# Kernel tuning notes

Hardware: AMD Instinct MI355X
Metric: run time of the kernel (lower is better)

The kernel has to match this reference:

```python
import jax, jax.numpy as jnp
import numpy as np


def setup_inputs() -> dict:
    key = jax.random.key(0)
    k1, k2 = jax.random.split(key)
    B, S, N, M = 4, 4, 4096, 4096
    output_points = jax.random.normal(k1, (B, S, N, 3), dtype=jnp.float32)
    target_points = jax.random.normal(k2, (B, S, M, 3), dtype=jnp.float32)
    return {"output_points": output_points, "target_points": target_points, "n_samples": 4096}


def reference(output_points, target_points, n_samples):
    # output_points: [B,S,N,3], target_points: [B,S,M,3] (already sampled to n_samples pts)
    x2 = jnp.sum(output_points * output_points, axis=-1)  # [B,S,N]
    y2 = jnp.sum(target_points * target_points, axis=-1)  # [B,S,M]
    xy = jnp.einsum('bsnd,bsmd->bsnm', output_points, target_points)  # [B,S,N,M]
    # squared pairwise distances; clamp tiny negatives from fp error
    d2 = jnp.maximum(x2[..., :, None] + y2[..., None, :] - 2.0 * xy, 0.0)
    dist1 = jnp.min(d2, axis=-1)  # [B,S,N] NN dist output->target (squared)
    dist2 = jnp.min(d2, axis=-2)  # [B,S,M] NN dist target->output (squared)
    # dist_combined per (b,s) = mean(dist1) + mean(dist2); tensor is [S,B]
    chamfer = jnp.mean(dist1, axis=-1) + jnp.mean(dist2, axis=-1)  # [B,S]
    return chamfer.T  # [n_future_steps, batch_size]
```

## Files before the change

### kernel.cpp

```cpp
#include <hip/hip_runtime.h>


constexpr int B = 4, S = 4, NPTS = 4096, PAIRS = B * S;
constexpr int THREADS = 1024;
constexpr int WAVES = THREADS / 64;
constexpr int QPT = 8;
constexpr int QPB = 64 * QPT;
constexpr int QTILES = NPTS / QPB;
constexpr int SEG = NPTS / WAVES;

typedef float v2f __attribute__((ext_vector_type(2)));

#define PK_FMA_ZW(g, q, rzw)                                              \
  asm("v_pk_fma_f32 %0, %1, %2, %2 op_sel:[0,0,1] op_sel_hi:[1,0,1]"      \
      : "=v"(g) : "v"(q), "v"(rzw))
#define PK_FMA_Y(g, q, rxy)                                               \
  asm("v_pk_fma_f32 %0, %1, %2, %0 op_sel:[0,1,0] op_sel_hi:[1,1,1]"      \
      : "+v"(g) : "v"(q), "v"(rxy))
#define PK_FMA_X(g, q, rxy)                                               \
  asm("v_pk_fma_f32 %0, %1, %2, %0 op_sel:[0,0,0] op_sel_hi:[1,0,1]"      \
      : "+v"(g) : "v"(q), "v"(rxy))

__global__ __launch_bounds__(THREADS, 4)
void chamfer_pk3_kernel(const float* __restrict__ out_pts,
                        const float* __restrict__ tgt_pts,
                        float* __restrict__ out) {
  const int t     = threadIdx.x;
  const int l     = t & 63;
  const int wid   = t >> 6;
  const int qtile = blockIdx.x;
  const int pair  = blockIdx.y;
  const int dir   = blockIdx.z;

  const float* qbase = (dir == 0 ? out_pts : tgt_pts) + (size_t)pair * NPTS * 3;
  const float* rbase = (dir == 0 ? tgt_pts : out_pts) + (size_t)pair * NPTS * 3;

  __shared__ float4 sref[NPTS];

  #pragma unroll
  for (int k = 0; k < NPTS / THREADS; ++k) {
    const int i = t + k * THREADS;
    const float rx = rbase[3 * i], ry = rbase[3 * i + 1], rz = rbase[3 * i + 2];
    sref[i] = make_float4(rx, ry, rz, -0.5f * (rx * rx + ry * ry + rz * rz));
  }

  v2f qx[4], qy[4], qz[4];
  #pragma unroll
  for (int p = 0; p < 4; ++p) {
    const int q0 = qtile * QPB + (2 * p) * 64 + l;
    const int q1 = q0 + 64;
    qx[p] = v2f{qbase[3 * q0], qbase[3 * q1]};
    qy[p] = v2f{qbase[3 * q0 + 1], qbase[3 * q1 + 1]};
    qz[p] = v2f{qbase[3 * q0 + 2], qbase[3 * q1 + 2]};
  }

  float acc[QPT];
  #pragma unroll
  for (int j = 0; j < QPT; ++j) acc[j] = -3.0e38f;

  __syncthreads();

  const int base = wid * SEG;
  #pragma unroll 2
  for (int r = 0; r < SEG; r += 2) {
    const float4 rf0 = sref[base + r];
    const float4 rf1 = sref[base + r + 1];
    v2f rxy0; rxy0.x = rf0.x; rxy0.y = rf0.y;
    v2f rzw0; rzw0.x = rf0.z; rzw0.y = rf0.w;
    v2f rxy1; rxy1.x = rf1.x; rxy1.y = rf1.y;
    v2f rzw1; rzw1.x = rf1.z; rzw1.y = rf1.w;
    #pragma unroll
    for (int p = 0; p < 4; ++p) {
      v2f g0, g1;
      PK_FMA_ZW(g0, qz[p], rzw0);
      PK_FMA_Y (g0, qy[p], rxy0);
      PK_FMA_X (g0, qx[p], rxy0);
      PK_FMA_ZW(g1, qz[p], rzw1);
      PK_FMA_Y (g1, qy[p], rxy1);
      PK_FMA_X (g1, qx[p], rxy1);
      acc[2 * p]     = fmaxf(fmaxf(acc[2 * p], g0.x), g1.x);
      acc[2 * p + 1] = fmaxf(fmaxf(acc[2 * p + 1], g0.y), g1.y);
    }
  }

  __syncthreads();
  float* Sf = reinterpret_cast<float*>(sref);

  #pragma unroll
  for (int j = 0; j < QPT; ++j) Sf[wid * QPB + j * 64 + l] = acc[j];
  __syncthreads();

  if (t < QPB) {
    float g = Sf[t];
    #pragma unroll
    for (int w = 1; w < WAVES; ++w) g = fmaxf(g, Sf[w * QPB + t]);
    const int j = t >> 6, p = j >> 1, h = j & 1;
    const float x2 = qx[p][h] * qx[p][h] + qy[p][h] * qy[p][h] + qz[p][h] * qz[p][h];
    float d = fmaxf(fmaf(-2.0f, g, x2), 0.0f);
    #pragma unroll
    for (int off = 1; off < 64; off <<= 1) d += __shfl_xor(d, off, 64);
    if (l == 0) Sf[WAVES * QPB + (t >> 6)] = d;
  }
  __syncthreads();
  if (t == 0) {
    float ssum = 0.0f;
    #pragma unroll
    for (int w = 0; w < QPB / 64; ++w) ssum += Sf[WAVES * QPB + w];
    const int b = pair >> 2, s = pair & 3;
    atomicAdd(&out[s * B + b], ssum * (1.0f / NPTS));
  }
}

extern "C" void kernel_launch(void* const* d_in, const int* in_sizes, int n_in,
                              void* d_out, int out_size, void* d_ws, size_t ws_size,
                              hipStream_t stream) {
  const float* out_pts = (const float*)d_in[0];
  const float* tgt_pts = (const float*)d_in[1];
  float* out = (float*)d_out;

  hipMemsetAsync(out, 0, out_size * sizeof(float), stream);
  dim3 grid(QTILES, PAIRS, 2);
  chamfer_pk3_kernel<<<grid, THREADS, 0, stream>>>(out_pts, tgt_pts, out);
}
```

Baseline: 99.23 us.

## Compute pairwise dot products with bf16 split-precision MFMA and two-pass reduction

Replaces the packed-FP32 VALU inner loop with 16x16x32 bf16 MFMA instructions. Each coordinate is split into three bf16 terms (hi/mid/lo) so the products approximate fp32 accuracy, and the -0.5*|r|^2 term is folded into the K dimension. Reference points are also split into four chunks across blocks; per-chunk maxima go to a workspace and a second finalize kernel combines them. This trades VALU FMA throughput for matrix-core throughput, at the cost of an extra launch, workspace traffic, and possible precision loss from the bf16 splitting.

```diff
diff --git a/kernel.cpp b/kernel.cpp
--- a/kernel.cpp
+++ b/kernel.cpp
@@ -2,110 +2,188 @@
 
 
 constexpr int B = 4, S = 4, NPTS = 4096, PAIRS = B * S;
-constexpr int THREADS = 1024;
+constexpr int UNITS = PAIRS * 2;
+constexpr int THREADS = 512;
 constexpr int WAVES = THREADS / 64;
-constexpr int QPT = 8;
-constexpr int QPB = 64 * QPT;
-constexpr int QTILES = NPTS / QPB;
-constexpr int SEG = NPTS / WAVES;
-
-typedef float v2f __attribute__((ext_vector_type(2)));
-
-#define PK_FMA_ZW(g, q, rzw)                                              \
-  asm("v_pk_fma_f32 %0, %1, %2, %2 op_sel:[0,0,1] op_sel_hi:[1,0,1]"      \
-      : "=v"(g) : "v"(q), "v"(rzw))
-#define PK_FMA_Y(g, q, rxy)                                               \
-  asm("v_pk_fma_f32 %0, %1, %2, %0 op_sel:[0,1,0] op_sel_hi:[1,1,1]"      \
-      : "+v"(g) : "v"(q), "v"(rxy))
-#define PK_FMA_X(g, q, rxy)                                               \
-  asm("v_pk_fma_f32 %0, %1, %2, %0 op_sel:[0,0,0] op_sel_hi:[1,0,1]"      \
-      : "+v"(g) : "v"(q), "v"(rxy))
+constexpr int AFRAGS = 8;
+constexpr int QPB = WAVES * AFRAGS * 16;
+constexpr int QCH = NPTS / QPB;
+constexpr int RCH = 4;
+constexpr int RPB = NPTS / RCH;
+constexpr int RTILES = RPB / 16;
+constexpr unsigned short BF16_ONE = 0x3F80;
+
+typedef __attribute__((ext_vector_type(8))) short bf16x8;
+typedef __attribute__((ext_vector_type(4))) float f32x4;
+typedef __attribute__((ext_vector_type(4))) unsigned int u32x4;
+
+static __device__ inline unsigned short bf16_rne(float v) {
+  unsigned int u = __builtin_bit_cast(unsigned int, v);
+  u += 0x7FFFu + ((u >> 16) & 1u);
+  return (unsigned short)(u >> 16);
+}
+static __device__ inline float bf16f(unsigned short h) {
+  unsigned int u = (unsigned int)h << 16;
+  return __builtin_bit_cast(float, u);
+}
+static __device__ inline unsigned int bpack(unsigned short lo, unsigned short hi) {
+  return (unsigned int)lo | ((unsigned int)hi << 16);
+}
+
+struct Split3 { unsigned short h, m, l; };
+static __device__ inline Split3 split3(float v) {
+  Split3 s;
+  s.h = bf16_rne(v);
+  float r = v - bf16f(s.h);
+  s.m = bf16_rne(r);
+  r -= bf16f(s.m);
+  s.l = bf16_rne(r);
+  return s;
+}
+
 
 __global__ __launch_bounds__(THREADS, 4)
-void chamfer_pk3_kernel(const float* __restrict__ out_pts,
-                        const float* __restrict__ tgt_pts,
-                        float* __restrict__ out) {
-  const int t     = threadIdx.x;
-  const int l     = t & 63;
-  const int wid   = t >> 6;
-  const int qtile = blockIdx.x;
-  const int pair  = blockIdx.y;
-  const int dir   = blockIdx.z;
-
-  const float* qbase = (dir == 0 ? out_pts : tgt_pts) + (size_t)pair * NPTS * 3;
-  const float* rbase = (dir == 0 ? tgt_pts : out_pts) + (size_t)pair * NPTS * 3;
-
-  __shared__ float4 sref[NPTS];
-
-  #pragma unroll
-  for (int k = 0; k < NPTS / THREADS; ++k) {
-    const int i = t + k * THREADS;
-    const float rx = rbase[3 * i], ry = rbase[3 * i + 1], rz = rbase[3 * i + 2];
-    sref[i] = make_float4(rx, ry, rz, -0.5f * (rx * rx + ry * ry + rz * rz));
-  }
-
-  v2f qx[4], qy[4], qz[4];
-  #pragma unroll
-  for (int p = 0; p < 4; ++p) {
-    const int q0 = qtile * QPB + (2 * p) * 64 + l;
-    const int q1 = q0 + 64;
-    qx[p] = v2f{qbase[3 * q0], qbase[3 * q1]};
-    qy[p] = v2f{qbase[3 * q0 + 1], qbase[3 * q1 + 1]};
-    qz[p] = v2f{qbase[3 * q0 + 2], qbase[3 * q1 + 2]};
-  }
-
-  float acc[QPT];
-  #pragma unroll
-  for (int j = 0; j < QPT; ++j) acc[j] = -3.0e38f;
-
-  __syncthreads();
-
-  const int base = wid * SEG;
-  #pragma unroll 2
-  for (int r = 0; r < SEG; r += 2) {
-    const float4 rf0 = sref[base + r];
-    const float4 rf1 = sref[base + r + 1];
-    v2f rxy0; rxy0.x = rf0.x; rxy0.y = rf0.y;
-    v2f rzw0; rzw0.x = rf0.z; rzw0.y = rf0.w;
-    v2f rxy1; rxy1.x = rf1.x; rxy1.y = rf1.y;
-    v2f rzw1; rzw1.x = rf1.z; rzw1.y = rf1.w;
-    #pragma unroll
-    for (int p = 0; p < 4; ++p) {
-      v2f g0, g1;
-      PK_FMA_ZW(g0, qz[p], rzw0);
-      PK_FMA_Y (g0, qy[p], rxy0);
-      PK_FMA_X (g0, qx[p], rxy0);
-      PK_FMA_ZW(g1, qz[p], rzw1);
-      PK_FMA_Y (g1, qy[p], rxy1);
-      PK_FMA_X (g1, qx[p], rxy1);
-      acc[2 * p]     = fmaxf(fmaxf(acc[2 * p], g0.x), g1.x);
-      acc[2 * p + 1] = fmaxf(fmaxf(acc[2 * p + 1], g0.y), g1.y);
-    }
-  }
-
-  __syncthreads();
-  float* Sf = reinterpret_cast<float*>(sref);
-
-  #pragma unroll
-  for (int j = 0; j < QPT; ++j) Sf[wid * QPB + j * 64 + l] = acc[j];
-  __syncthreads();
-
-  if (t < QPB) {
-    float g = Sf[t];
-    #pragma unroll
-    for (int w = 1; w < WAVES; ++w) g = fmaxf(g, Sf[w * QPB + t]);
-    const int j = t >> 6, p = j >> 1, h = j & 1;
-    const float x2 = qx[p][h] * qx[p][h] + qy[p][h] * qy[p][h] + qz[p][h] * qz[p][h];
-    float d = fmaxf(fmaf(-2.0f, g, x2), 0.0f);
-    #pragma unroll
-    for (int off = 1; off < 64; off <<= 1) d += __shfl_xor(d, off, 64);
-    if (l == 0) Sf[WAVES * QPB + (t >> 6)] = d;
-  }
+void chamfer_mfma_main(const float* __restrict__ out_pts,
+                       const float* __restrict__ tgt_pts,
+                       float* __restrict__ part) {
+  const int t = threadIdx.x;
+  const int l = t & 63;
+  const int wid = t >> 6;
+  const int qc = blockIdx.x;
+  const int rc = blockIdx.y;
+  const int unit = blockIdx.z;
+  const int pair = unit >> 1, dir = unit & 1;
+
+  const float* qpts = (dir == 0 ? out_pts : tgt_pts) + (size_t)pair * NPTS * 3;
+  const float* rpts = (dir == 0 ? tgt_pts : out_pts) + (size_t)pair * NPTS * 3;
+
+  __shared__ u32x4 lds[RTILES * 64];
+
+  {
+    const int q0 = qc * QPB;
+    #pragma unroll
+    for (int rep = 0; rep < QPB / THREADS; ++rep) {
+      const int j = t + rep * THREADS;
+      const float x = qpts[3 * (q0 + j)];
+      const float y = qpts[3 * (q0 + j) + 1];
+      const float z = qpts[3 * (q0 + j) + 2];
+      const Split3 sx = split3(x), sy = split3(y), sz = split3(z);
+      u32x4* base = lds + (j >> 4) * 64 + (j & 15);
+      const u32x4 g0 = {bpack(sx.h, sx.h), bpack(sx.m, sx.h),
+                        bpack(sx.l, sx.m), bpack(sy.h, sy.h)};
+      const u32x4 g1 = {bpack(sy.m, sy.h), bpack(sy.l, sy.m),
+                        bpack(sz.h, sz.h), bpack(sz.m, sz.h)};
+      const u32x4 g2 = {bpack(sz.l, sz.m), bpack(BF16_ONE, BF16_ONE),
+                        bpack(BF16_ONE, 0), 0u};
+      const u32x4 g3 = {0u, 0u, 0u, 0u};
+      base[0] = g0; base[16] = g1; base[32] = g2; base[48] = g3;
+    }
+  }
+  __syncthreads();
+
+  bf16x8 a[AFRAGS];
+  #pragma unroll
+  for (int m = 0; m < AFRAGS; ++m)
+    a[m] = ((const bf16x8*)lds)[(wid * AFRAGS + m) * 64 + l];
+  __syncthreads();
+
+  {
+    const int r0 = rc * RPB;
+    #pragma unroll
+    for (int rep = 0; rep < RPB / THREADS; ++rep) {
+      const int j = t + rep * THREADS;
+      const float x = rpts[3 * (r0 + j)];
+      const float y = rpts[3 * (r0 + j) + 1];
+      const float z = rpts[3 * (r0 + j) + 2];
+      const float w = -0.5f * (x * x + y * y + z * z);
+      const Split3 sx = split3(x), sy = split3(y), sz = split3(z), sw = split3(w);
+      u32x4* base = lds + (j >> 4) * 64 + (j & 15);
+      const u32x4 g0 = {bpack(sx.h, sx.m), bpack(sx.h, sx.l),
+                        bpack(sx.h, sx.m), bpack(sy.h, sy.m)};
+      const u32x4 g1 = {bpack(sy.h, sy.l), bpack(sy.h, sy.m),
+                        bpack(sz.h, sz.m), bpack(sz.h, sz.l)};
+      const u32x4 g2 = {bpack(sz.h, sz.m), bpack(sw.h, sw.m),
+                        bpack(sw.l, 0), 0u};
+      const u32x4 g3 = {0u, 0u, 0u, 0u};
+      base[0] = g0; base[16] = g1; base[32] = g2; base[48] = g3;
+    }
+  }
+  __syncthreads();
+
+  f32x4 acc[AFRAGS];
+  #pragma unroll
+  for (int m = 0; m < AFRAGS; ++m)
+    acc[m] = (f32x4){-3.0e38f, -3.0e38f, -3.0e38f, -3.0e38f};
+
+  const f32x4 czero = {0.f, 0.f, 0.f, 0.f};
+  const bf16x8* bptr = (const bf16x8*)lds;
+  for (int tt = 0; tt < RTILES; tt += 2) {
+    const bf16x8 b0 = bptr[tt * 64 + l];
+    const bf16x8 b1 = bptr[(tt + 1) * 64 + l];
+    #pragma unroll
+    for (int m = 0; m < AFRAGS; ++m) {
+      const f32x4 d0 = __builtin_amdgcn_mfma_f32_16x16x32_bf16(a[m], b0, czero, 0, 0, 0);
+      const f32x4 d1 = __builtin_amdgcn_mfma_f32_16x16x32_bf16(a[m], b1, czero, 0, 0, 0);
+      #pragma unroll
+      for (int c = 0; c < 4; ++c)
+        acc[m][c] = fmaxf(fmaxf(acc[m][c], d0[c]), d1[c]);
+    }
+  }
+
+  #pragma unroll
+  for (int m = 0; m < AFRAGS; ++m) {
+    #pragma unroll
+    for (int c = 0; c < 4; ++c) {
+      float g = acc[m][c];
+      g = fmaxf(g, __shfl_xor(g, 1, 64));
+      g = fmaxf(g, __shfl_xor(g, 2, 64));
+      g = fmaxf(g, __shfl_xor(g, 4, 64));
+      g = fmaxf(g, __shfl_xor(g, 8, 64));
+      acc[m][c] = g;
+    }
+  }
+  const int jj = l & 15, hi = l >> 4;
+  float v_lo = 0.f, v_hi = 0.f;
+  #pragma unroll
+  for (int m = 0; m < 4; ++m) {
+    #pragma unroll
+    for (int c = 0; c < 4; ++c) {
+      const bool sel = (jj == m * 4 + c);
+      v_lo = sel ? acc[m][c] : v_lo;
+      v_hi = sel ? acc[m + 4][c] : v_hi;
+    }
+  }
+  const int q = qc * QPB + wid * (AFRAGS * 16) + (jj >> 2) * 16 + hi * 4 + (jj & 3);
+  float* pdst = part + ((size_t)unit * NPTS + q) * RCH + rc;
+  pdst[0] = v_lo;
+  pdst[64 * RCH] = v_hi;
+}
+
+__global__ __launch_bounds__(256)
+void chamfer_finalize(const float* __restrict__ out_pts,
+                      const float* __restrict__ tgt_pts,
+                      const float* __restrict__ part,
+                      float* __restrict__ out) {
+  const int t = threadIdx.x;
+  const int blk = blockIdx.x;
+  const int unit = blk >> 4;
+  const int q = (blk & 15) * 256 + t;
+  const int pair = unit >> 1, dir = unit & 1;
+  const float* qpts = (dir == 0 ? out_pts : tgt_pts) + (size_t)pair * NPTS * 3;
+
+  const f32x4 p = *(const f32x4*)(part + ((size_t)unit * NPTS + q) * RCH);
+  const float g = fmaxf(fmaxf(p[0], p[1]), fmaxf(p[2], p[3]));
+  const float x = qpts[3 * q], y = qpts[3 * q + 1], z = qpts[3 * q + 2];
+  const float x2 = x * x + y * y + z * z;
+  float d = fmaxf(fmaf(-2.0f, g, x2), 0.0f);
+
+  #pragma unroll
+  for (int off = 1; off < 64; off <<= 1) d += __shfl_xor(d, off, 64);
+  __shared__ float sum4[4];
+  if ((t & 63) == 0) sum4[t >> 6] = d;
   __syncthreads();
   if (t == 0) {
-    float ssum = 0.0f;
-    #pragma unroll
-    for (int w = 0; w < QPB / 64; ++w) ssum += Sf[WAVES * QPB + w];
+    const float ssum = (sum4[0] + sum4[1]) + (sum4[2] + sum4[3]);
     const int b = pair >> 2, s = pair & 3;
     atomicAdd(&out[s * B + b], ssum * (1.0f / NPTS));
   }
@@ -114,11 +192,14 @@
 extern "C" void kernel_launch(void* const* d_in, const int* in_sizes, int n_in,
                               void* d_out, int out_size, void* d_ws, size_t ws_size,
                               hipStream_t stream) {
+  (void)in_sizes; (void)n_in; (void)ws_size;
   const float* out_pts = (const float*)d_in[0];
   const float* tgt_pts = (const float*)d_in[1];
   float* out = (float*)d_out;
+  float* part = (float*)d_ws;
 
   hipMemsetAsync(out, 0, out_size * sizeof(float), stream);
-  dim3 grid(QTILES, PAIRS, 2);
-  chamfer_pk3_kernel<<<grid, THREADS, 0, stream>>>(out_pts, tgt_pts, out);
-}
+  dim3 grid(QCH, RCH, UNITS);
+  chamfer_mfma_main<<<grid, THREADS, 0, stream>>>(out_pts, tgt_pts, part);
+  chamfer_finalize<<<dim3(UNITS * 16), 256, 0, stream>>>(out_pts, tgt_pts, part, out);
+}
```

After: 92.34 us. 1.07x faster.
